# Kernel optimization log

Hardware: AMD Instinct MI355X
Metric: run time of the kernel (lower is better)

## Reference

```python
import jax, jax.numpy as jnp
import numpy as np

N, NFEAT, NHID, NHID2 = 10000, 512, 256, 128


def setup_inputs() -> dict:
    key = jax.random.key(0)
    k1, k2, k3, k4 = jax.random.split(key, 4)
    x = jax.random.normal(k1, (N, NFEAT), dtype=jnp.float32)
    # sparse-ish row-normalized adjacency, stored dense (as the module's spmm operand)
    raw = jax.random.uniform(k2, (N, N), dtype=jnp.float32)
    adj = jnp.where(raw > 0.995, raw, 0.0)
    adj = adj / jnp.maximum(adj.sum(axis=1, keepdims=True), 1e-6)
    W1 = jax.random.normal(k3, (NFEAT, NHID), dtype=jnp.float32) / np.sqrt(NFEAT)
    b1 = jnp.zeros((NHID,), dtype=jnp.float32)
    W2 = jax.random.normal(k4, (NHID, NHID2), dtype=jnp.float32) / np.sqrt(NHID)
    b2 = jnp.zeros((NHID2,), dtype=jnp.float32)
    return {"x": x, "adj": adj, "W1": W1, "b1": b1, "W2": W2, "b2": b2}


def gcn_conv(x, adj, W, b):
    # standard Kipf GCNConv: adj @ (x @ W) + b
    return adj @ (x @ W) + b


def reference(x, adj, W1, b1, W2, b2):
    h = jax.nn.relu(gcn_conv(x, adj, W1, b1))
    # dropout is identity in inference mode (training=False)
    h = jax.nn.relu(gcn_conv(h, adj, W2, b2))
    return h
```

## Files before the change

### kernel.cpp

```cpp
#include <hip/hip_runtime.h>

#define N_NODES 10000
#define NFEAT   512
#define NHID    256
#define NHID2   128
#define CAP     128

typedef __attribute__((ext_vector_type(8))) short bf16x8;
typedef __attribute__((ext_vector_type(4))) float f32x4;

__device__ __forceinline__ ushort f2bf(float f){
  union { float f; unsigned u; } v; v.f = f;
  unsigned r = v.u + 0x7FFFu + ((v.u >> 16) & 1u);
  return (ushort)(r >> 16);
}
__device__ __forceinline__ float bf2f(ushort u){
  union { unsigned u; float f; } v; v.u = ((unsigned)u) << 16; return v.f;
}

__global__ void k_cvt_all(const float* __restrict__ x, const float* __restrict__ W1,
                          const float* __restrict__ W2, ushort* __restrict__ xb,
                          ushort* __restrict__ w1t, ushort* __restrict__ w2t){
  const int b = blockIdx.x, t = threadIdx.x;
  if (b < 5000){
    int i = (b * 256 + t) * 4;
    float4 q = *(const float4*)(x + i);
    ushort4 o; o.x = f2bf(q.x); o.y = f2bf(q.y); o.z = f2bf(q.z); o.w = f2bf(q.w);
    *(ushort4*)(xb + i) = o;
  } else if (b < 5512){
    int id = (b - 5000) * 256 + t;
    int n = id >> 9, k = id & 511;
    w1t[id] = f2bf(W1[k * NHID + n]);
  } else {
    int id = (b - 5512) * 256 + t;
    int n = id >> 8, k = id & 255;
    w2t[id] = f2bf(W2[k * NHID2 + n]);
  }
}

template<int WR, int WC, bool OUT_BF16>
__launch_bounds__(256)
__global__ void k_gemm_bf16(const ushort* __restrict__ A, const ushort* __restrict__ Bt,
                            void* __restrict__ Cv, int M, int N, int K){
  const int lane = threadIdx.x & 63;
  const int w    = threadIdx.x >> 6;
  const int wr   = w >> 1, wc = w & 1;
  const int r16  = lane & 15;
  const int kg   = lane >> 4;
  const int BM = 2 * WR * 16, BN = 2 * WC * 16;
  const int row0 = blockIdx.x * BM + wr * WR * 16;
  const int col0 = blockIdx.y * BN + wc * WC * 16;

  f32x4 acc[WR][WC];
  #pragma unroll
  for (int r = 0; r < WR; r++)
    #pragma unroll
    for (int c = 0; c < WC; c++)
      acc[r][c] = (f32x4){0.f, 0.f, 0.f, 0.f};

  for (int k0 = 0; k0 < K; k0 += 32){
    bf16x8 a[WR], b[WC];
    #pragma unroll
    for (int r = 0; r < WR; r++){
      int ar = row0 + r * 16 + r16;
      if (ar >= M) ar = M - 1;
      a[r] = *(const bf16x8*)(A + (size_t)ar * K + k0 + kg * 8);
    }
    #pragma unroll
    for (int c = 0; c < WC; c++){
      int bc = col0 + c * 16 + r16;
      b[c] = *(const bf16x8*)(Bt + (size_t)bc * K + k0 + kg * 8);
    }
    #pragma unroll
    for (int r = 0; r < WR; r++)
      #pragma unroll
      for (int c = 0; c < WC; c++)
        acc[r][c] = __builtin_amdgcn_mfma_f32_16x16x32_bf16(a[r], b[c], acc[r][c], 0, 0, 0);
  }

  #pragma unroll
  for (int r = 0; r < WR; r++)
    #pragma unroll
    for (int c = 0; c < WC; c++){
      int col = col0 + c * 16 + r16;
      #pragma unroll
      for (int i = 0; i < 4; i++){
        int row = row0 + r * 16 + kg * 4 + i;
        if (row < M){
          if (OUT_BF16) ((ushort*)Cv)[(size_t)row * N + col] = f2bf(acc[r][c][i]);
          else          ((float*) Cv)[(size_t)row * N + col] = acc[r][c][i];
        }
      }
    }
}

__launch_bounds__(256)
__global__ void k_spmm1(const float* __restrict__ adj, const ushort* __restrict__ xw1b,
                        const float* __restrict__ b1, ushort* __restrict__ Hb,
                        int* __restrict__ row_nnz, int2* __restrict__ pja){
  const int r = blockIdx.x;
  const int t = threadIdx.x;
  const int lane = t & 63, w = t >> 6;
  const float* row = adj + (size_t)r * N_NODES;

  __shared__ int   swave[4];
  __shared__ int   lj[CAP];
  __shared__ float la[CAP];
  __shared__ float part[8 * NHID];

  float4 vals[10];
  #pragma unroll
  for (int v = 0; v < 9; v++)
    vals[v] = *(const float4*)(row + v * 1024 + t * 4);
  vals[9] = (float4){0.f, 0.f, 0.f, 0.f};
  if (t < 196) vals[9] = *(const float4*)(row + 9216 + t * 4);

  int cnt = 0;
  #pragma unroll
  for (int v = 0; v < 10; v++)
    cnt += (vals[v].x != 0.f) + (vals[v].y != 0.f) + (vals[v].z != 0.f) + (vals[v].w != 0.f);

  int incl = cnt;
  #pragma unroll
  for (int d = 1; d < 64; d <<= 1){
    int u = __shfl_up(incl, d, 64);
    if (lane >= d) incl += u;
  }
  if (lane == 63) swave[w] = incl;
  __syncthreads();
  int woff = 0, total = 0;
  #pragma unroll
  for (int i = 0; i < 4; i++){
    int s = swave[i];
    total += s;
    if (i < w) woff += s;
  }
  int pos = woff + incl - cnt;

  #pragma unroll
  for (int v = 0; v < 10; v++){
    float q[4] = {vals[v].x, vals[v].y, vals[v].z, vals[v].w};
    #pragma unroll
    for (int e = 0; e < 4; e++){
      if (q[e] != 0.f && pos < CAP){
        int idx = v * 1024 + t * 4 + e;
        lj[pos] = idx; la[pos] = q[e];
        pja[(size_t)r * CAP + pos] = make_int2(idx, __float_as_int(q[e]));
        pos++;
      }
    }
  }
  __syncthreads();
  const int n = min(total, CAP);
  if (t == 0) row_nnz[r] = n;

  const int slot = w * 2 + (lane >> 5);
  const int l32  = lane & 31;
  float accv[8] = {0.f,0.f,0.f,0.f,0.f,0.f,0.f,0.f};
  for (int k = slot; k < n; k += 8){
    bf16x8 rv = *(const bf16x8*)(xw1b + (size_t)lj[k] * NHID + l32 * 8);
    float a = la[k];
    #pragma unroll
    for (int j = 0; j < 8; j++)
      accv[j] += a * bf2f((ushort)rv[j]);
  }
  #pragma unroll
  for (int j = 0; j < 8; j++)
    part[slot * NHID + l32 * 8 + j] = accv[j];
  __syncthreads();

  float s = 0.f;
  #pragma unroll
  for (int i = 0; i < 8; i++)
    s += part[i * NHID + t];
  Hb[(size_t)r * NHID + t] = f2bf(fmaxf(s + b1[t], 0.f));
}

__launch_bounds__(256)
__global__ void k_spmm2(const int* __restrict__ row_nnz, const int2* __restrict__ pja,
                        const float* __restrict__ hw2, const float* __restrict__ b2,
                        float* __restrict__ out){
  const int r = blockIdx.x;
  const int t = threadIdx.x;
  __shared__ int   lj[CAP];
  __shared__ float la[CAP];
  __shared__ float part[8 * NHID2];
  const int n = row_nnz[r];
  if (t < n){
    int2 p = pja[(size_t)r * CAP + t];
    lj[t] = p.x; la[t] = __int_as_float(p.y);
  }
  __syncthreads();

  const int lane = t & 63, w = t >> 6;
  const int slot = w * 2 + (lane >> 5);
  const int l32  = lane & 31;
  float4 accv = (float4){0.f,0.f,0.f,0.f};
  for (int k = slot; k < n; k += 8){
    float4 rv = *(const float4*)(hw2 + (size_t)lj[k] * NHID2 + l32 * 4);
    float a = la[k];
    accv.x += a * rv.x; accv.y += a * rv.y; accv.z += a * rv.z; accv.w += a * rv.w;
  }
  *(float4*)(part + slot * NHID2 + l32 * 4) = accv;
  __syncthreads();

  if (t < NHID2){
    float s = 0.f;
    #pragma unroll
    for (int i = 0; i < 8; i++)
      s += part[i * NHID2 + t];
    out[(size_t)r * NHID2 + t] = fmaxf(s + b2[t], 0.f);
  }
}

extern "C" void kernel_launch(void* const* d_in, const int* in_sizes, int n_in,
                              void* d_out, int out_size, void* d_ws, size_t ws_size,
                              hipStream_t stream){
  const float* x   = (const float*)d_in[0];
  const float* adj = (const float*)d_in[1];
  const float* W1  = (const float*)d_in[2];
  const float* b1  = (const float*)d_in[3];
  const float* W2  = (const float*)d_in[4];
  const float* b2  = (const float*)d_in[5];
  float* out = (float*)d_out;
  char*  ws  = (char*)d_ws;

  ushort* xb   = (ushort*)(ws);
  ushort* w1t  = (ushort*)(ws + 10240000);
  ushort* w2t  = (ushort*)(ws + 10502144);
  ushort* xw1b = (ushort*)(ws + 10567680);
  ushort* Hb   = (ushort*)(ws + 15687680);
  float*  hw2  = (float*)(ws + 20807680);
  int*    nnz  = (int*)(ws + 25927680);
  int2*   pja  = (int2*)(ws + 25967680);

  k_cvt_all<<<5640, 256, 0, stream>>>(x, W1, W2, xb, w1t, w2t);

  k_gemm_bf16<4,2,true><<<dim3(79, 4), 256, 0, stream>>>(xb, w1t, xw1b, N_NODES, NHID, NFEAT);

  k_spmm1<<<N_NODES, 256, 0, stream>>>(adj, xw1b, b1, Hb, nnz, pja);

  k_gemm_bf16<2,2,false><<<dim3(157, 2), 256, 0, stream>>>(Hb, w2t, hw2, N_NODES, NHID2, NHID);

  k_spmm2<<<N_NODES, 256, 0, stream>>>(nnz, pja, hw2, b2, out);
}
```

Baseline: 157.1 us.

## Move adjacency scan into conversion kernel, double-buffer GEMM loads, bf16 hw2

The dense adjacency scan and compaction now run in the same launch as the x/W conversion, so the 400MB adj read no longer waits behind the first GEMM and is split out of the first aggregation. The GEMM gets a compile-time K, precomputed row and column offsets, and a two-stage register double buffer of fragment loads. The second GEMM now writes bf16, and the second aggregation gathers bf16 rows with 16 slots. The cost is an extra kernel that rereads the compacted lists and reduced precision for the hw2 intermediate.

```diff
diff --git a/kernel.cpp b/kernel.cpp
--- a/kernel.cpp
+++ b/kernel.cpp
@@ -18,30 +18,84 @@
   union { unsigned u; float f; } v; v.u = ((unsigned)u) << 16; return v.f;
 }
 
-__global__ void k_cvt_all(const float* __restrict__ x, const float* __restrict__ W1,
-                          const float* __restrict__ W2, ushort* __restrict__ xb,
-                          ushort* __restrict__ w1t, ushort* __restrict__ w2t){
+__launch_bounds__(256)
+__global__ void k_scan_cvt(const float* __restrict__ adj, const float* __restrict__ x,
+                           const float* __restrict__ W1, const float* __restrict__ W2,
+                           ushort* __restrict__ xb, ushort* __restrict__ w1t,
+                           ushort* __restrict__ w2t, int* __restrict__ row_nnz,
+                           int2* __restrict__ pja){
   const int b = blockIdx.x, t = threadIdx.x;
-  if (b < 5000){
-    int i = (b * 256 + t) * 4;
-    float4 q = *(const float4*)(x + i);
-    ushort4 o; o.x = f2bf(q.x); o.y = f2bf(q.y); o.z = f2bf(q.z); o.w = f2bf(q.w);
-    *(ushort4*)(xb + i) = o;
-  } else if (b < 5512){
-    int id = (b - 5000) * 256 + t;
-    int n = id >> 9, k = id & 511;
-    w1t[id] = f2bf(W1[k * NHID + n]);
-  } else {
-    int id = (b - 5512) * 256 + t;
-    int n = id >> 8, k = id & 255;
-    w2t[id] = f2bf(W2[k * NHID2 + n]);
-  }
-}
-
-template<int WR, int WC, bool OUT_BF16>
-__launch_bounds__(256)
-__global__ void k_gemm_bf16(const ushort* __restrict__ A, const ushort* __restrict__ Bt,
-                            void* __restrict__ Cv, int M, int N, int K){
+
+  if (b >= N_NODES){
+    if (b < 15000){
+      int i = ((b - N_NODES) * 256 + t) * 4;
+      float4 q = *(const float4*)(x + i);
+      ushort4 o; o.x = f2bf(q.x); o.y = f2bf(q.y); o.z = f2bf(q.z); o.w = f2bf(q.w);
+      *(ushort4*)(xb + i) = o;
+    } else if (b < 15512){
+      int id = (b - 15000) * 256 + t;
+      int n = id >> 9, k = id & 511;
+      w1t[id] = f2bf(W1[k * NHID + n]);
+    } else {
+      int id = (b - 15512) * 256 + t;
+      int n = id >> 8, k = id & 255;
+      w2t[id] = f2bf(W2[k * NHID2 + n]);
+    }
+    return;
+  }
+
+  const int r = b;
+  const int lane = t & 63, w = t >> 6;
+  const float* row = adj + (size_t)r * N_NODES;
+  __shared__ int swave[4];
+
+  float4 vals[10];
+  #pragma unroll
+  for (int v = 0; v < 9; v++)
+    vals[v] = *(const float4*)(row + v * 1024 + t * 4);
+  vals[9] = (float4){0.f, 0.f, 0.f, 0.f};
+  if (t < 196) vals[9] = *(const float4*)(row + 9216 + t * 4);
+
+  int cnt = 0;
+  #pragma unroll
+  for (int v = 0; v < 10; v++)
+    cnt += (vals[v].x != 0.f) + (vals[v].y != 0.f) + (vals[v].z != 0.f) + (vals[v].w != 0.f);
+
+  int incl = cnt;
+  #pragma unroll
+  for (int d = 1; d < 64; d <<= 1){
+    int u = __shfl_up(incl, d, 64);
+    if (lane >= d) incl += u;
+  }
+  if (lane == 63) swave[w] = incl;
+  __syncthreads();
+  int woff = 0, total = 0;
+  #pragma unroll
+  for (int i = 0; i < 4; i++){
+    int s = swave[i];
+    total += s;
+    if (i < w) woff += s;
+  }
+  int pos = woff + incl - cnt;
+
+  #pragma unroll
+  for (int v = 0; v < 10; v++){
+    float q[4] = {vals[v].x, vals[v].y, vals[v].z, vals[v].w};
+    #pragma unroll
+    for (int e = 0; e < 4; e++){
+      if (q[e] != 0.f && pos < CAP){
+        pja[(size_t)r * CAP + pos] = make_int2(v * 1024 + t * 4 + e, __float_as_int(q[e]));
+        pos++;
+      }
+    }
+  }
+  if (t == 0) row_nnz[r] = min(total, CAP);
+}
+
+template<int WR, int WC, bool OUT_BF16, int K>
+__launch_bounds__(256)
+__global__ void k_gemm(const ushort* __restrict__ A, const ushort* __restrict__ Bt,
+                       void* __restrict__ Cv, int M, int N){
   const int lane = threadIdx.x & 63;
   const int w    = threadIdx.x >> 6;
   const int wr   = w >> 1, wc = w & 1;
@@ -51,6 +105,15 @@
   const int row0 = blockIdx.x * BM + wr * WR * 16;
   const int col0 = blockIdx.y * BN + wc * WC * 16;
 
+  int arow[WR], bcol[WC];
+  #pragma unroll
+  for (int r = 0; r < WR; r++){
+    int ar = row0 + r * 16 + r16;
+    arow[r] = (ar >= M) ? (M - 1) : ar;
+  }
+  #pragma unroll
+  for (int c = 0; c < WC; c++) bcol[c] = col0 + c * 16 + r16;
+
   f32x4 acc[WR][WC];
   #pragma unroll
   for (int r = 0; r < WR; r++)
@@ -58,24 +121,30 @@
     for (int c = 0; c < WC; c++)
       acc[r][c] = (f32x4){0.f, 0.f, 0.f, 0.f};
 
-  for (int k0 = 0; k0 < K; k0 += 32){
-    bf16x8 a[WR], b[WC];
-    #pragma unroll
-    for (int r = 0; r < WR; r++){
-      int ar = row0 + r * 16 + r16;
-      if (ar >= M) ar = M - 1;
-      a[r] = *(const bf16x8*)(A + (size_t)ar * K + k0 + kg * 8);
-    }
-    #pragma unroll
-    for (int c = 0; c < WC; c++){
-      int bc = col0 + c * 16 + r16;
-      b[c] = *(const bf16x8*)(Bt + (size_t)bc * K + k0 + kg * 8);
-    }
+  bf16x8 aA[WR], bA[WC], aB[WR], bB[WC];
+  auto LOADF = [&](bf16x8* a, bf16x8* b, int k0){
+    #pragma unroll
+    for (int r = 0; r < WR; r++)
+      a[r] = *(const bf16x8*)(A + (size_t)arow[r] * K + k0 + kg * 8);
+    #pragma unroll
+    for (int c = 0; c < WC; c++)
+      b[c] = *(const bf16x8*)(Bt + (size_t)bcol[c] * K + k0 + kg * 8);
+  };
+  auto MM = [&](bf16x8* a, bf16x8* b){
     #pragma unroll
     for (int r = 0; r < WR; r++)
       #pragma unroll
       for (int c = 0; c < WC; c++)
         acc[r][c] = __builtin_amdgcn_mfma_f32_16x16x32_bf16(a[r], b[c], acc[r][c], 0, 0, 0);
+  };
+
+  LOADF(aA, bA, 0);
+  #pragma unroll
+  for (int k0 = 0; k0 < K; k0 += 64){
+    if (k0 + 32 < K) LOADF(aB, bB, k0 + 32);
+    MM(aA, bA);
+    if (k0 + 64 < K) LOADF(aA, bA, k0 + 64);
+    if (k0 + 32 < K) MM(aB, bB);
   }
 
   #pragma unroll
@@ -95,67 +164,21 @@
 }
 
 __launch_bounds__(256)
-__global__ void k_spmm1(const float* __restrict__ adj, const ushort* __restrict__ xw1b,
-                        const float* __restrict__ b1, ushort* __restrict__ Hb,
-                        int* __restrict__ row_nnz, int2* __restrict__ pja){
-  const int r = blockIdx.x;
-  const int t = threadIdx.x;
-  const int lane = t & 63, w = t >> 6;
-  const float* row = adj + (size_t)r * N_NODES;
-
-  __shared__ int   swave[4];
+__global__ void k_agg1(const int* __restrict__ row_nnz, const int2* __restrict__ pja,
+                       const ushort* __restrict__ xw1b, const float* __restrict__ b1,
+                       ushort* __restrict__ Hb){
+  const int r = blockIdx.x, t = threadIdx.x;
   __shared__ int   lj[CAP];
   __shared__ float la[CAP];
   __shared__ float part[8 * NHID];
-
-  float4 vals[10];
-  #pragma unroll
-  for (int v = 0; v < 9; v++)
-    vals[v] = *(const float4*)(row + v * 1024 + t * 4);
-  vals[9] = (float4){0.f, 0.f, 0.f, 0.f};
-  if (t < 196) vals[9] = *(const float4*)(row + 9216 + t * 4);
-
-  int cnt = 0;
-  #pragma unroll
-  for (int v = 0; v < 10; v++)
-    cnt += (vals[v].x != 0.f) + (vals[v].y != 0.f) + (vals[v].z != 0.f) + (vals[v].w != 0.f);
-
-  int incl = cnt;
-  #pragma unroll
-  for (int d = 1; d < 64; d <<= 1){
-    int u = __shfl_up(incl, d, 64);
-    if (lane >= d) incl += u;
-  }
-  if (lane == 63) swave[w] = incl;
-  __syncthreads();
-  int woff = 0, total = 0;
-  #pragma unroll
-  for (int i = 0; i < 4; i++){
-    int s = swave[i];
-    total += s;
-    if (i < w) woff += s;
-  }
-  int pos = woff + incl - cnt;
-
-  #pragma unroll
-  for (int v = 0; v < 10; v++){
-    float q[4] = {vals[v].x, vals[v].y, vals[v].z, vals[v].w};
-    #pragma unroll
-    for (int e = 0; e < 4; e++){
-      if (q[e] != 0.f && pos < CAP){
-        int idx = v * 1024 + t * 4 + e;
-        lj[pos] = idx; la[pos] = q[e];
-        pja[(size_t)r * CAP + pos] = make_int2(idx, __float_as_int(q[e]));
-        pos++;
-      }
-    }
-  }
-  __syncthreads();
-  const int n = min(total, CAP);
-  if (t == 0) row_nnz[r] = n;
-
-  const int slot = w * 2 + (lane >> 5);
-  const int l32  = lane & 31;
+  const int n = row_nnz[r];
+  if (t < n){
+    int2 p = pja[(size_t)r * CAP + t];
+    lj[t] = p.x; la[t] = __int_as_float(p.y);
+  }
+  __syncthreads();
+
+  const int slot = t >> 5, l32 = t & 31;
   float accv[8] = {0.f,0.f,0.f,0.f,0.f,0.f,0.f,0.f};
   for (int k = slot; k < n; k += 8){
     bf16x8 rv = *(const bf16x8*)(xw1b + (size_t)lj[k] * NHID + l32 * 8);
@@ -177,14 +200,13 @@
 }
 
 __launch_bounds__(256)
-__global__ void k_spmm2(const int* __restrict__ row_nnz, const int2* __restrict__ pja,
-                        const float* __restrict__ hw2, const float* __restrict__ b2,
-                        float* __restrict__ out){
-  const int r = blockIdx.x;
-  const int t = threadIdx.x;
+__global__ void k_agg2(const int* __restrict__ row_nnz, const int2* __restrict__ pja,
+                       const ushort* __restrict__ hw2b, const float* __restrict__ b2,
+                       float* __restrict__ out){
+  const int r = blockIdx.x, t = threadIdx.x;
   __shared__ int   lj[CAP];
   __shared__ float la[CAP];
-  __shared__ float part[8 * NHID2];
+  __shared__ float part[16 * NHID2];
   const int n = row_nnz[r];
   if (t < n){
     int2 p = pja[(size_t)r * CAP + t];
@@ -192,22 +214,24 @@
   }
   __syncthreads();
 
-  const int lane = t & 63, w = t >> 6;
-  const int slot = w * 2 + (lane >> 5);
-  const int l32  = lane & 31;
-  float4 accv = (float4){0.f,0.f,0.f,0.f};
-  for (int k = slot; k < n; k += 8){
-    float4 rv = *(const float4*)(hw2 + (size_t)lj[k] * NHID2 + l32 * 4);
+  const int slot = t >> 4, l16 = t & 15;
+  float accv[8] = {0.f,0.f,0.f,0.f,0.f,0.f,0.f,0.f};
+  for (int k = slot; k < n; k += 16){
+    bf16x8 rv = *(const bf16x8*)(hw2b + (size_t)lj[k] * NHID2 + l16 * 8);
     float a = la[k];
-    accv.x += a * rv.x; accv.y += a * rv.y; accv.z += a * rv.z; accv.w += a * rv.w;
-  }
-  *(float4*)(part + slot * NHID2 + l32 * 4) = accv;
+    #pragma unroll
+    for (int j = 0; j < 8; j++)
+      accv[j] += a * bf2f((ushort)rv[j]);
+  }
+  #pragma unroll
+  for (int j = 0; j < 8; j++)
+    part[slot * NHID2 + l16 * 8 + j] = accv[j];
   __syncthreads();
 
   if (t < NHID2){
     float s = 0.f;
     #pragma unroll
-    for (int i = 0; i < 8; i++)
+    for (int i = 0; i < 16; i++)
       s += part[i * NHID2 + t];
     out[(size_t)r * NHID2 + t] = fmaxf(s + b2[t], 0.f);
   }
@@ -230,17 +254,17 @@
   ushort* w2t  = (ushort*)(ws + 10502144);
   ushort* xw1b = (ushort*)(ws + 10567680);
   ushort* Hb   = (ushort*)(ws + 15687680);
-  float*  hw2  = (float*)(ws + 20807680);
-  int*    nnz  = (int*)(ws + 25927680);
-  int2*   pja  = (int2*)(ws + 25967680);
-
-  k_cvt_all<<<5640, 256, 0, stream>>>(x, W1, W2, xb, w1t, w2t);
-
-  k_gemm_bf16<4,2,true><<<dim3(79, 4), 256, 0, stream>>>(xb, w1t, xw1b, N_NODES, NHID, NFEAT);
-
-  k_spmm1<<<N_NODES, 256, 0, stream>>>(adj, xw1b, b1, Hb, nnz, pja);
-
-  k_gemm_bf16<2,2,false><<<dim3(157, 2), 256, 0, stream>>>(Hb, w2t, hw2, N_NODES, NHID2, NHID);
-
-  k_spmm2<<<N_NODES, 256, 0, stream>>>(nnz, pja, hw2, b2, out);
-}
+  ushort* hw2b = (ushort*)(ws + 20807680);
+  int*    nnz  = (int*)(ws + 23367680);
+  int2*   pja  = (int2*)(ws + 23407680);
+
+  k_scan_cvt<<<15640, 256, 0, stream>>>(adj, x, W1, W2, xb, w1t, w2t, nnz, pja);
+
+  k_gemm<4,2,true,NFEAT><<<dim3(79, 4), 256, 0, stream>>>(xb, w1t, xw1b, N_NODES, NHID);
+
+  k_agg1<<<N_NODES, 256, 0, stream>>>(nnz, pja, xw1b, b1, Hb);
+
+  k_gemm<2,2,true,NHID><<<dim3(157, 2), 256, 0, stream>>>(Hb, w2t, hw2b, N_NODES, NHID2);
+
+  k_agg2<<<N_NODES, 256, 0, stream>>>(nnz, pja, hw2b, b2, out);
+}
```

Result: no change. 156.8 us (-0.2%).

## Fuse adjacency scan with first GEMM and split aggregation into half-width passes

Applied to the files above, without the earlier changes.

Merges the dense-adjacency nonzero scan and the X·W1 GEMM into one launch, with separate block ranges doing each job, so the memory-bound scan can overlap the compute-bound GEMM. The first aggregation is split into two 128-column passes over half-width bf16 tables to shrink the gathered working set, and hW2 is stored as bf16 instead of fp32. The GEMMs get smaller 64x64 tiles with software double-buffered loads, and adjacency and pja reads use nontemporal loads. The cost is an extra aggregation launch, re-reading the pja lists, and slightly lower precision in the second layer's gathered table.

```diff
diff --git a/kernel.cpp b/kernel.cpp
--- a/kernel.cpp
+++ b/kernel.cpp
@@ -8,6 +8,7 @@
 
 typedef __attribute__((ext_vector_type(8))) short bf16x8;
 typedef __attribute__((ext_vector_type(4))) float f32x4;
+typedef __attribute__((ext_vector_type(2))) int   i32x2;
 
 __device__ __forceinline__ ushort f2bf(float f){
   union { float f; unsigned u; } v; v.f = f;
@@ -18,9 +19,9 @@
   union { unsigned u; float f; } v; v.u = ((unsigned)u) << 16; return v.f;
 }
 
-__global__ void k_cvt_all(const float* __restrict__ x, const float* __restrict__ W1,
-                          const float* __restrict__ W2, ushort* __restrict__ xb,
-                          ushort* __restrict__ w1t, ushort* __restrict__ w2t){
+__global__ void k_cvt(const float* __restrict__ x, const float* __restrict__ W1,
+                      const float* __restrict__ W2, ushort* __restrict__ xb,
+                      ushort* __restrict__ w1t, ushort* __restrict__ w2t){
   const int b = blockIdx.x, t = threadIdx.x;
   if (b < 5000){
     int i = (b * 256 + t) * 4;
@@ -38,179 +39,231 @@
   }
 }
 
-template<int WR, int WC, bool OUT_BF16>
 __launch_bounds__(256)
-__global__ void k_gemm_bf16(const ushort* __restrict__ A, const ushort* __restrict__ Bt,
-                            void* __restrict__ Cv, int M, int N, int K){
+__global__ void k_scan_gemm1(const float* __restrict__ adj, const ushort* __restrict__ xb,
+                             const ushort* __restrict__ w1t, ushort* __restrict__ xw1_lo,
+                             ushort* __restrict__ xw1_hi, int* __restrict__ row_nnz,
+                             i32x2* __restrict__ pja){
+  const int b = blockIdx.x, t = threadIdx.x;
+  const int lane = t & 63, w = t >> 6;
+
+  if (b < 628){
+    const int bx = b % 157, by = b / 157;
+    const int wr = w >> 1, wc = w & 1;
+    const int r16 = lane & 15, kg = lane >> 4;
+    const int row0 = bx * 64 + wr * 32;
+    const int col0 = by * 64 + wc * 32;
+
+    int arow[2], bcol[2];
+    #pragma unroll
+    for (int r = 0; r < 2; r++){
+      int ar = row0 + r * 16 + r16;
+      arow[r] = (ar >= N_NODES) ? (N_NODES - 1) : ar;
+    }
+    #pragma unroll
+    for (int c = 0; c < 2; c++) bcol[c] = col0 + c * 16 + r16;
+
+    f32x4 acc[2][2];
+    #pragma unroll
+    for (int r = 0; r < 2; r++)
+      #pragma unroll
+      for (int c = 0; c < 2; c++)
+        acc[r][c] = (f32x4){0.f, 0.f, 0.f, 0.f};
+
+    bf16x8 aA[2], bA[2], aB[2], bB[2];
+    auto LOADF = [&](bf16x8* a, bf16x8* bb, int k0){
+      #pragma unroll
+      for (int r = 0; r < 2; r++)
+        a[r] = *(const bf16x8*)(xb + (size_t)arow[r] * NFEAT + k0 + kg * 8);
+      #pragma unroll
+      for (int c = 0; c < 2; c++)
+        bb[c] = *(const bf16x8*)(w1t + (size_t)bcol[c] * NFEAT + k0 + kg * 8);
+    };
+    auto MM = [&](bf16x8* a, bf16x8* bb){
+      #pragma unroll
+      for (int r = 0; r < 2; r++)
+        #pragma unroll
+        for (int c = 0; c < 2; c++)
+          acc[r][c] = __builtin_amdgcn_mfma_f32_16x16x32_bf16(a[r], bb[c], acc[r][c], 0, 0, 0);
+    };
+
+    LOADF(aA, bA, 0);
+    #pragma unroll
+    for (int k0 = 0; k0 < NFEAT; k0 += 64){
+      if (k0 + 32 < NFEAT) LOADF(aB, bB, k0 + 32);
+      MM(aA, bA);
+      if (k0 + 64 < NFEAT) LOADF(aA, bA, k0 + 64);
+      if (k0 + 32 < NFEAT) MM(aB, bB);
+    }
+
+    ushort* dst = (by < 2) ? xw1_lo : xw1_hi;
+    const int cbase = (by < 2) ? 0 : 128;
+    #pragma unroll
+    for (int r = 0; r < 2; r++)
+      #pragma unroll
+      for (int c = 0; c < 2; c++){
+        int col = col0 + c * 16 + r16 - cbase;
+        #pragma unroll
+        for (int i = 0; i < 4; i++){
+          int row = row0 + r * 16 + kg * 4 + i;
+          if (row < N_NODES) dst[(size_t)row * 128 + col] = f2bf(acc[r][c][i]);
+        }
+      }
+    return;
+  }
+
+  const int r = b - 628;
+  const float* row = adj + (size_t)r * N_NODES;
+  __shared__ int swave[4];
+
+  f32x4 vals[10];
+  #pragma unroll
+  for (int v = 0; v < 9; v++)
+    vals[v] = __builtin_nontemporal_load((const f32x4*)(row + v * 1024 + t * 4));
+  vals[9] = (f32x4){0.f, 0.f, 0.f, 0.f};
+  if (t < 196) vals[9] = __builtin_nontemporal_load((const f32x4*)(row + 9216 + t * 4));
+
+  int cnt = 0;
+  #pragma unroll
+  for (int v = 0; v < 10; v++)
+    cnt += (vals[v].x != 0.f) + (vals[v].y != 0.f) + (vals[v].z != 0.f) + (vals[v].w != 0.f);
+
+  int incl = cnt;
+  #pragma unroll
+  for (int d = 1; d < 64; d <<= 1){
+    int u = __shfl_up(incl, d, 64);
+    if (lane >= d) incl += u;
+  }
+  if (lane == 63) swave[w] = incl;
+  __syncthreads();
+  int woff = 0, total = 0;
+  #pragma unroll
+  for (int i = 0; i < 4; i++){
+    int s = swave[i];
+    total += s;
+    if (i < w) woff += s;
+  }
+  int pos = woff + incl - cnt;
+
+  #pragma unroll
+  for (int v = 0; v < 10; v++){
+    float q[4] = {vals[v].x, vals[v].y, vals[v].z, vals[v].w};
+    #pragma unroll
+    for (int e = 0; e < 4; e++){
+      if (q[e] != 0.f && pos < CAP){
+        pja[(size_t)r * CAP + pos] = (i32x2){v * 1024 + t * 4 + e, __float_as_int(q[e])};
+        pos++;
+      }
+    }
+  }
+  if (t == 0) row_nnz[r] = min(total, CAP);
+}
+
+template<bool TO_BF16, int DS>
+__launch_bounds__(256)
+__global__ void k_agg_half(const int* __restrict__ row_nnz, const i32x2* __restrict__ pja,
+                           const ushort* __restrict__ table, const float* __restrict__ bias,
+                           void* __restrict__ dst){
+  const int r = blockIdx.x, t = threadIdx.x;
+  __shared__ int   lj[CAP];
+  __shared__ float la[CAP];
+  __shared__ float part[16 * 128];
+  const int n = row_nnz[r];
+  if (t < n){
+    i32x2 p = __builtin_nontemporal_load(pja + (size_t)r * CAP + t);
+    lj[t] = p.x; la[t] = __int_as_float(p.y);
+  }
+  __syncthreads();
+
+  const int slot = t >> 4, l16 = t & 15;
+  float accv[8] = {0.f,0.f,0.f,0.f,0.f,0.f,0.f,0.f};
+  for (int k = slot; k < n; k += 16){
+    bf16x8 rv = *(const bf16x8*)(table + (size_t)lj[k] * 128 + l16 * 8);
+    float a = la[k];
+    #pragma unroll
+    for (int j = 0; j < 8; j++)
+      accv[j] += a * bf2f((ushort)rv[j]);
+  }
+  #pragma unroll
+  for (int j = 0; j < 8; j++)
+    part[slot * 128 + l16 * 8 + j] = accv[j];
+  __syncthreads();
+
+  if (t < 128){
+    float s = 0.f;
+    #pragma unroll
+    for (int i = 0; i < 16; i++)
+      s += part[i * 128 + t];
+    s = fmaxf(s + bias[t], 0.f);
+    if (TO_BF16) ((ushort*)dst)[(size_t)r * DS + t] = f2bf(s);
+    else         ((float*) dst)[(size_t)r * DS + t] = s;
+  }
+}
+
+__launch_bounds__(256)
+__global__ void k_gemm2(const ushort* __restrict__ A, const ushort* __restrict__ Bt,
+                        ushort* __restrict__ C){
   const int lane = threadIdx.x & 63;
   const int w    = threadIdx.x >> 6;
   const int wr   = w >> 1, wc = w & 1;
   const int r16  = lane & 15;
   const int kg   = lane >> 4;
-  const int BM = 2 * WR * 16, BN = 2 * WC * 16;
-  const int row0 = blockIdx.x * BM + wr * WR * 16;
-  const int col0 = blockIdx.y * BN + wc * WC * 16;
-
-  f32x4 acc[WR][WC];
-  #pragma unroll
-  for (int r = 0; r < WR; r++)
-    #pragma unroll
-    for (int c = 0; c < WC; c++)
+  const int row0 = blockIdx.x * 64 + wr * 32;
+  const int col0 = blockIdx.y * 64 + wc * 32;
+
+  int arow[2], bcol[2];
+  #pragma unroll
+  for (int r = 0; r < 2; r++){
+    int ar = row0 + r * 16 + r16;
+    arow[r] = (ar >= N_NODES) ? (N_NODES - 1) : ar;
+  }
+  #pragma unroll
+  for (int c = 0; c < 2; c++) bcol[c] = col0 + c * 16 + r16;
+
+  f32x4 acc[2][2];
+  #pragma unroll
+  for (int r = 0; r < 2; r++)
+    #pragma unroll
+    for (int c = 0; c < 2; c++)
       acc[r][c] = (f32x4){0.f, 0.f, 0.f, 0.f};
 
-  for (int k0 = 0; k0 < K; k0 += 32){
-    bf16x8 a[WR], b[WC];
-    #pragma unroll
-    for (int r = 0; r < WR; r++){
-      int ar = row0 + r * 16 + r16;
-      if (ar >= M) ar = M - 1;
-      a[r] = *(const bf16x8*)(A + (size_t)ar * K + k0 + kg * 8);
-    }
-    #pragma unroll
-    for (int c = 0; c < WC; c++){
-      int bc = col0 + c * 16 + r16;
-      b[c] = *(const bf16x8*)(Bt + (size_t)bc * K + k0 + kg * 8);
-    }
-    #pragma unroll
-    for (int r = 0; r < WR; r++)
-      #pragma unroll
-      for (int c = 0; c < WC; c++)
-        acc[r][c] = __builtin_amdgcn_mfma_f32_16x16x32_bf16(a[r], b[c], acc[r][c], 0, 0, 0);
-  }
-
-  #pragma unroll
-  for (int r = 0; r < WR; r++)
-    #pragma unroll
-    for (int c = 0; c < WC; c++){
+  bf16x8 aA[2], bA[2], aB[2], bB[2];
+  auto LOADF = [&](bf16x8* a, bf16x8* bb, int k0){
+    #pragma unroll
+    for (int r = 0; r < 2; r++)
+      a[r] = *(const bf16x8*)(A + (size_t)arow[r] * NHID + k0 + kg * 8);
+    #pragma unroll
+    for (int c = 0; c < 2; c++)
+      bb[c] = *(const bf16x8*)(Bt + (size_t)bcol[c] * NHID + k0 + kg * 8);
+  };
+  auto MM = [&](bf16x8* a, bf16x8* bb){
+    #pragma unroll
+    for (int r = 0; r < 2; r++)
+      #pragma unroll
+      for (int c = 0; c < 2; c++)
+        acc[r][c] = __builtin_amdgcn_mfma_f32_16x16x32_bf16(a[r], bb[c], acc[r][c], 0, 0, 0);
+  };
+
+  LOADF(aA, bA, 0);
+  #pragma unroll
+  for (int k0 = 0; k0 < NHID; k0 += 64){
+    if (k0 + 32 < NHID) LOADF(aB, bB, k0 + 32);
+    MM(aA, bA);
+    if (k0 + 64 < NHID) LOADF(aA, bA, k0 + 64);
+    if (k0 + 32 < NHID) MM(aB, bB);
+  }
+
+  #pragma unroll
+  for (int r = 0; r < 2; r++)
+    #pragma unroll
+    for (int c = 0; c < 2; c++){
       int col = col0 + c * 16 + r16;
       #pragma unroll
       for (int i = 0; i < 4; i++){
         int row = row0 + r * 16 + kg * 4 + i;
-        if (row < M){
-          if (OUT_BF16) ((ushort*)Cv)[(size_t)row * N + col] = f2bf(acc[r][c][i]);
-          else          ((float*) Cv)[(size_t)row * N + col] = acc[r][c][i];
-        }
+        if (row < N_NODES) C[(size_t)row * NHID2 + col] = f2bf(acc[r][c][i]);
       }
     }
-}
-
-__launch_bounds__(256)
-__global__ void k_spmm1(const float* __restrict__ adj, const ushort* __restrict__ xw1b,
-                        const float* __restrict__ b1, ushort* __restrict__ Hb,
-                        int* __restrict__ row_nnz, int2* __restrict__ pja){
-  const int r = blockIdx.x;
-  const int t = threadIdx.x;
-  const int lane = t & 63, w = t >> 6;
-  const float* row = adj + (size_t)r * N_NODES;
-
-  __shared__ int   swave[4];
-  __shared__ int   lj[CAP];
-  __shared__ float la[CAP];
-  __shared__ float part[8 * NHID];
-
-  float4 vals[10];
-  #pragma unroll
-  for (int v = 0; v < 9; v++)
-    vals[v] = *(const float4*)(row + v * 1024 + t * 4);
-  vals[9] = (float4){0.f, 0.f, 0.f, 0.f};
-  if (t < 196) vals[9] = *(const float4*)(row + 9216 + t * 4);
-
-  int cnt = 0;
-  #pragma unroll
-  for (int v = 0; v < 10; v++)
-    cnt += (vals[v].x != 0.f) + (vals[v].y != 0.f) + (vals[v].z != 0.f) + (vals[v].w != 0.f);
-
-  int incl = cnt;
-  #pragma unroll
-  for (int d = 1; d < 64; d <<= 1){
-    int u = __shfl_up(incl, d, 64);
-    if (lane >= d) incl += u;
-  }
-  if (lane == 63) swave[w] = incl;
-  __syncthreads();
-  int woff = 0, total = 0;
-  #pragma unroll
-  for (int i = 0; i < 4; i++){
-    int s = swave[i];
-    total += s;
-    if (i < w) woff += s;
-  }
-  int pos = woff + incl - cnt;
-
-  #pragma unroll
-  for (int v = 0; v < 10; v++){
-    float q[4] = {vals[v].x, vals[v].y, vals[v].z, vals[v].w};
-    #pragma unroll
-    for (int e = 0; e < 4; e++){
-      if (q[e] != 0.f && pos < CAP){
-        int idx = v * 1024 + t * 4 + e;
-        lj[pos] = idx; la[pos] = q[e];
-        pja[(size_t)r * CAP + pos] = make_int2(idx, __float_as_int(q[e]));
-        pos++;
-      }
-    }
-  }
-  __syncthreads();
-  const int n = min(total, CAP);
-  if (t == 0) row_nnz[r] = n;
-
-  const int slot = w * 2 + (lane >> 5);
-  const int l32  = lane & 31;
-  float accv[8] = {0.f,0.f,0.f,0.f,0.f,0.f,0.f,0.f};
-  for (int k = slot; k < n; k += 8){
-    bf16x8 rv = *(const bf16x8*)(xw1b + (size_t)lj[k] * NHID + l32 * 8);
-    float a = la[k];
-    #pragma unroll
-    for (int j = 0; j < 8; j++)
-      accv[j] += a * bf2f((ushort)rv[j]);
-  }
-  #pragma unroll
-  for (int j = 0; j < 8; j++)
-    part[slot * NHID + l32 * 8 + j] = accv[j];
-  __syncthreads();
-
-  float s = 0.f;
-  #pragma unroll
-  for (int i = 0; i < 8; i++)
-    s += part[i * NHID + t];
-  Hb[(size_t)r * NHID + t] = f2bf(fmaxf(s + b1[t], 0.f));
-}
-
-__launch_bounds__(256)
-__global__ void k_spmm2(const int* __restrict__ row_nnz, const int2* __restrict__ pja,
-                        const float* __restrict__ hw2, const float* __restrict__ b2,
-                        float* __restrict__ out){
-  const int r = blockIdx.x;
-  const int t = threadIdx.x;
-  __shared__ int   lj[CAP];
-  __shared__ float la[CAP];
-  __shared__ float part[8 * NHID2];
-  const int n = row_nnz[r];
-  if (t < n){
-    int2 p = pja[(size_t)r * CAP + t];
-    lj[t] = p.x; la[t] = __int_as_float(p.y);
-  }
-  __syncthreads();
-
-  const int lane = t & 63, w = t >> 6;
-  const int slot = w * 2 + (lane >> 5);
-  const int l32  = lane & 31;
-  float4 accv = (float4){0.f,0.f,0.f,0.f};
-  for (int k = slot; k < n; k += 8){
-    float4 rv = *(const float4*)(hw2 + (size_t)lj[k] * NHID2 + l32 * 4);
-    float a = la[k];
-    accv.x += a * rv.x; accv.y += a * rv.y; accv.z += a * rv.z; accv.w += a * rv.w;
-  }
-  *(float4*)(part + slot * NHID2 + l32 * 4) = accv;
-  __syncthreads();
-
-  if (t < NHID2){
-    float s = 0.f;
-    #pragma unroll
-    for (int i = 0; i < 8; i++)
-      s += part[i * NHID2 + t];
-    out[(size_t)r * NHID2 + t] = fmaxf(s + b2[t], 0.f);
-  }
 }
 
 extern "C" void kernel_launch(void* const* d_in, const int* in_sizes, int n_in,
@@ -225,22 +278,24 @@
   float* out = (float*)d_out;
   char*  ws  = (char*)d_ws;
 
-  ushort* xb   = (ushort*)(ws);
-  ushort* w1t  = (ushort*)(ws + 10240000);
-  ushort* w2t  = (ushort*)(ws + 10502144);
-  ushort* xw1b = (ushort*)(ws + 10567680);
-  ushort* Hb   = (ushort*)(ws + 15687680);
-  float*  hw2  = (float*)(ws + 20807680);
-  int*    nnz  = (int*)(ws + 25927680);
-  int2*   pja  = (int2*)(ws + 25967680);
-
-  k_cvt_all<<<5640, 256, 0, stream>>>(x, W1, W2, xb, w1t, w2t);
-
-  k_gemm_bf16<4,2,true><<<dim3(79, 4), 256, 0, stream>>>(xb, w1t, xw1b, N_NODES, NHID, NFEAT);
-
-  k_spmm1<<<N_NODES, 256, 0, stream>>>(adj, xw1b, b1, Hb, nnz, pja);
-
-  k_gemm_bf16<2,2,false><<<dim3(157, 2), 256, 0, stream>>>(Hb, w2t, hw2, N_NODES, NHID2, NHID);
-
-  k_spmm2<<<N_NODES, 256, 0, stream>>>(nnz, pja, hw2, b2, out);
-}
+  ushort* xb     = (ushort*)(ws);
+  ushort* w1t    = (ushort*)(ws + 10240000);
+  ushort* w2t    = (ushort*)(ws + 10502144);
+  ushort* xw1_lo = (ushort*)(ws + 10567680);
+  ushort* xw1_hi = (ushort*)(ws + 13127680);
+  ushort* Hb     = (ushort*)(ws + 15687680);
+  ushort* hw2b   = (ushort*)(ws + 20807680);
+  int*    nnz    = (int*)(ws + 23367680);
+  i32x2*  pja    = (i32x2*)(ws + 23407680);
+
+  k_cvt<<<5640, 256, 0, stream>>>(x, W1, W2, xb, w1t, w2t);
+
+  k_scan_gemm1<<<10628, 256, 0, stream>>>(adj, xb, w1t, xw1_lo, xw1_hi, nnz, pja);
+
+  k_agg_half<true, NHID><<<N_NODES, 256, 0, stream>>>(nnz, pja, xw1_lo, b1,       Hb);
+  k_agg_half<true, NHID><<<N_NODES, 256, 0, stream>>>(nnz, pja, xw1_hi, b1 + 128, Hb + 128);
+
+  k_gemm2<<<dim3(157, 2), 256, 0, stream>>>(Hb, w2t, hw2b);
+
+  k_agg_half<false, NHID2><<<N_NODES, 256, 0, stream>>>(nnz, pja, hw2b, b2, out);
+}
```

Result: no change. 154.2 us (-1.8%).
